# Performance work log

Hardware: AMD Instinct MI355X
Metric: run time of the kernel (lower is better)

## Reference

```python
import jax, jax.numpy as jnp
import numpy as np

H, KB = 8, 8          # z_num grid (h, k)
OB, IB = 64, 64       # per-call weight block [OB, IB, K]
K, L = 9, 9           # kernel dims of exe_unet_weight and unet_1d_weights
ZD, PD, DH = 64, 16, 128  # z_dim, pde_inputs dim, hypernet hidden


def setup_inputs() -> dict:
    key = jax.random.key(0)
    k1, k2, k3, k4, k5 = jax.random.split(key, 5)
    # z params: torch.fmod(randn, 2) as in the original __init__
    z_all = jnp.fmod(jax.random.normal(k1, (H * KB, ZD), jnp.float32), 2.0)
    W1 = jax.random.normal(k2, (DH, ZD + PD), jnp.float32) * 0.1
    b1 = jnp.zeros((DH,), jnp.float32)
    W2 = jax.random.normal(k3, (OB * IB * K, DH), jnp.float32) * 0.02
    b2 = jnp.zeros((OB * IB * K,), jnp.float32)
    unet_1d_weights = jax.random.normal(k4, (H * OB, KB * IB, L), jnp.float32)
    pde_inputs = jax.random.normal(k5, (PD,), jnp.float32)
    return {"z_all": z_all, "W1": W1, "b1": b1, "W2": W2, "b2": b2,
            "unet_1d_weights": unet_1d_weights, "pde_inputs": pde_inputs}


def reference(z_all, W1, b1, W2, b2, unet_1d_weights, pde_inputs):
    # Batched hypernet: one GEMM over all h*k z vectors instead of h*k calls.
    x = jnp.concatenate([z_all, jnp.broadcast_to(pde_inputs, (H * KB, PD))], axis=1)  # [hk, ZD+PD]
    hid = jax.nn.relu(x @ W1.T + b1)                    # [hk, DH]
    w = (hid @ W2.T + b2).reshape(H, KB, OB, IB, K)      # per-cell blocks
    # cat(dim=1) within row, cat(dim=0) across rows -> [H*OB, KB*IB, K]
    exe_unet_weight = w.transpose(0, 2, 1, 3, 4).reshape(H * OB, KB * IB, K)
    # broadcast outer product over kernel dims
    w_2d = jnp.einsum('oik,oil->oikl', exe_unet_weight, unet_1d_weights)
    return w_2d
```

## Files before the change

### kernel.cpp

```cpp
#include <hip/hip_runtime.h>

#define ZD_ 64
#define PD_ 16
#define DH_ 128
#define NW2 36864
#define HK_ 64
#define HK_TILE 8

__global__ void hid_kernel(const float* __restrict__ z_all,
                           const float* __restrict__ W1,
                           const float* __restrict__ b1,
                           const float* __restrict__ pde,
                           float* __restrict__ hid) {
    int gid = blockIdx.x * 256 + threadIdx.x;
    int r = gid >> 7;
    int d = gid & 127;
    const float* w = W1 + d * (ZD_ + PD_);
    const float* z = z_all + r * ZD_;
    float acc = b1[d];
    #pragma unroll 8
    for (int c = 0; c < ZD_; ++c) acc += z[c] * w[c];
    #pragma unroll
    for (int c = 0; c < PD_; ++c) acc += pde[c] * w[ZD_ + c];
    hid[gid] = fmaxf(acc, 0.0f);
}

__global__ void transpose_w2(const float* __restrict__ W2,
                             float* __restrict__ W2T) {
    __shared__ float s[32][33];
    int n0 = blockIdx.x * 32;
    int k0 = blockIdx.y * 32;
    int row = threadIdx.x >> 3;
    int c4  = (threadIdx.x & 7) * 4;
    float4 v = *reinterpret_cast<const float4*>(W2 + (size_t)(n0 + row) * DH_ + k0 + c4);
    s[row][c4 + 0] = v.x; s[row][c4 + 1] = v.y;
    s[row][c4 + 2] = v.z; s[row][c4 + 3] = v.w;
    __syncthreads();
    float4 w;
    w.x = s[c4 + 0][row]; w.y = s[c4 + 1][row];
    w.z = s[c4 + 2][row]; w.w = s[c4 + 3][row];
    *reinterpret_cast<float4*>(W2T + (size_t)(k0 + row) * NW2 + n0 + c4) = w;
}

__global__ void exe_kernel(const float* __restrict__ hid,
                           const float* __restrict__ W2T,
                           const float* __restrict__ b2,
                           float* __restrict__ exe) {
    int nblk = blockIdx.x % 72;
    int h    = blockIdx.x / 72;
    int n = nblk * 512 + threadIdx.x * 4;
    const float* hrow = hid + (size_t)h * HK_TILE * DH_;

    float4 bias = *reinterpret_cast<const float4*>(b2 + n);
    float4 acc[HK_TILE];
    #pragma unroll
    for (int j = 0; j < HK_TILE; ++j) acc[j] = bias;

    #pragma unroll 2
    for (int k = 0; k < DH_; k += 4) {
        float4 w0 = *reinterpret_cast<const float4*>(W2T + (size_t)(k + 0) * NW2 + n);
        float4 w1 = *reinterpret_cast<const float4*>(W2T + (size_t)(k + 1) * NW2 + n);
        float4 w2 = *reinterpret_cast<const float4*>(W2T + (size_t)(k + 2) * NW2 + n);
        float4 w3 = *reinterpret_cast<const float4*>(W2T + (size_t)(k + 3) * NW2 + n);
        #pragma unroll
        for (int j = 0; j < HK_TILE; ++j) {
            float4 hv = *reinterpret_cast<const float4*>(hrow + j * DH_ + k);
            acc[j].x += hv.x * w0.x; acc[j].y += hv.x * w0.y;
            acc[j].z += hv.x * w0.z; acc[j].w += hv.x * w0.w;
            acc[j].x += hv.y * w1.x; acc[j].y += hv.y * w1.y;
            acc[j].z += hv.y * w1.z; acc[j].w += hv.y * w1.w;
            acc[j].x += hv.z * w2.x; acc[j].y += hv.z * w2.y;
            acc[j].z += hv.z * w2.z; acc[j].w += hv.z * w2.w;
            acc[j].x += hv.w * w3.x; acc[j].y += hv.w * w3.y;
            acc[j].z += hv.w * w3.z; acc[j].w += hv.w * w3.w;
        }
    }

    int ob = n / 576;
    int r  = n % 576;
    #pragma unroll
    for (int j = 0; j < HK_TILE; ++j) {
        int o = h * 64 + ob;
        *reinterpret_cast<float4*>(exe + (size_t)o * 4608 + j * 576 + r) = acc[j];
    }
}

__global__ void outer_kernel(const float* __restrict__ exe,
                             const float* __restrict__ unet,
                             float* __restrict__ out) {
    __shared__ float s_e[576], s_u[576];
    int b = blockIdx.x;
    int o = b >> 3, c = b & 7;
    size_t base9 = (size_t)o * 4608 + (size_t)c * 576;
    const float4* e4 = reinterpret_cast<const float4*>(exe + base9);
    const float4* u4 = reinterpret_cast<const float4*>(unet + base9);
    int tid = threadIdx.x;
    if (tid < 144) {
        reinterpret_cast<float4*>(s_e)[tid] = e4[tid];
        reinterpret_cast<float4*>(s_u)[tid] = u4[tid];
    }
    __syncthreads();
    float4* o4 = reinterpret_cast<float4*>(out + (size_t)o * 41472 + (size_t)c * 5184);
    for (int idx = tid; idx < 1296; idx += 256) {
        int e0 = idx * 4;
        float4 v;
        float* vp = &v.x;
        #pragma unroll
        for (int j = 0; j < 4; ++j) {
            int e = e0 + j;
            int p = e / 81;
            int rem = e - p * 81;
            int k = rem / 9;
            int l = rem - k * 9;
            vp[j] = s_e[p * 9 + k] * s_u[p * 9 + l];
        }
        o4[idx] = v;
    }
}

extern "C" void kernel_launch(void* const* d_in, const int* in_sizes, int n_in,
                              void* d_out, int out_size, void* d_ws, size_t ws_size,
                              hipStream_t stream) {
    const float* z_all = (const float*)d_in[0];
    const float* W1    = (const float*)d_in[1];
    const float* b1    = (const float*)d_in[2];
    const float* W2    = (const float*)d_in[3];
    const float* b2    = (const float*)d_in[4];
    const float* unet  = (const float*)d_in[5];
    const float* pde   = (const float*)d_in[6];
    float* out = (float*)d_out;

    float* ws   = (float*)d_ws;
    float* hid  = ws;
    float* W2T  = ws + 8192;
    float* exe  = W2T + (size_t)DH_ * NW2;

    hid_kernel<<<32, 256, 0, stream>>>(z_all, W1, b1, pde, hid);
    transpose_w2<<<dim3(1152, 4), 256, 0, stream>>>(W2, W2T);
    exe_kernel<<<576, 128, 0, stream>>>(hid, W2T, b2, exe);
    outer_kernel<<<4096, 256, 0, stream>>>(exe, unet, out);
}
```

Baseline: 159.7 us.

## Drop W2 transpose pass; stage W2 tiles in LDS inside exe GEMM

Removes the separate transpose kernel that wrote an 18MB transposed copy of W2, and instead has each exe block load a 64-row slab of W2 into padded shared memory. Each wave computes 16 hk rows for 64 output columns, reading W2 from LDS and hid via broadcast loads. This cuts a full extra read/write pass over W2 and one launch. The trade-offs are LDS use per block, scalar rather than float4 stores to exe, and hid being re-read by every block.

```diff
diff --git a/kernel.cpp b/kernel.cpp
--- a/kernel.cpp
+++ b/kernel.cpp
@@ -3,9 +3,7 @@
 #define ZD_ 64
 #define PD_ 16
 #define DH_ 128
-#define NW2 36864
-#define HK_ 64
-#define HK_TILE 8
+#define LDS_STRIDE 132
 
 __global__ void hid_kernel(const float* __restrict__ z_all,
                            const float* __restrict__ W1,
@@ -25,63 +23,54 @@
     hid[gid] = fmaxf(acc, 0.0f);
 }
 
-__global__ void transpose_w2(const float* __restrict__ W2,
-                             float* __restrict__ W2T) {
-    __shared__ float s[32][33];
-    int n0 = blockIdx.x * 32;
-    int k0 = blockIdx.y * 32;
-    int row = threadIdx.x >> 3;
-    int c4  = (threadIdx.x & 7) * 4;
-    float4 v = *reinterpret_cast<const float4*>(W2 + (size_t)(n0 + row) * DH_ + k0 + c4);
-    s[row][c4 + 0] = v.x; s[row][c4 + 1] = v.y;
-    s[row][c4 + 2] = v.z; s[row][c4 + 3] = v.w;
+__global__ __launch_bounds__(256) void exe_kernel(
+        const float* __restrict__ hid,
+        const float* __restrict__ W2,
+        const float* __restrict__ b2,
+        float* __restrict__ exe) {
+    __shared__ __align__(16) float s_tile[64 * LDS_STRIDE];
+    int tid = threadIdx.x;
+    int n0  = blockIdx.x * 64;
+
+    const float4* g4 = reinterpret_cast<const float4*>(W2 + (size_t)n0 * DH_);
+    #pragma unroll
+    for (int j = 0; j < 8; ++j) {
+        int g  = j * 256 + tid;
+        int nl = g >> 5;
+        int k0 = (g & 31) * 4;
+        *reinterpret_cast<float4*>(&s_tile[nl * LDS_STRIDE + k0]) = g4[g];
+    }
     __syncthreads();
-    float4 w;
-    w.x = s[c4 + 0][row]; w.y = s[c4 + 1][row];
-    w.z = s[c4 + 2][row]; w.w = s[c4 + 3][row];
-    *reinterpret_cast<float4*>(W2T + (size_t)(k0 + row) * NW2 + n0 + c4) = w;
-}
 
-__global__ void exe_kernel(const float* __restrict__ hid,
-                           const float* __restrict__ W2T,
-                           const float* __restrict__ b2,
-                           float* __restrict__ exe) {
-    int nblk = blockIdx.x % 72;
-    int h    = blockIdx.x / 72;
-    int n = nblk * 512 + threadIdx.x * 4;
-    const float* hrow = hid + (size_t)h * HK_TILE * DH_;
+    int wave   = __builtin_amdgcn_readfirstlane(tid >> 6);
+    int lane   = tid & 63;
+    int hkbase = wave * 16;
+    const float* hbase = hid + (size_t)hkbase * DH_;
 
-    float4 bias = *reinterpret_cast<const float4*>(b2 + n);
-    float4 acc[HK_TILE];
+    float bias = b2[n0 + lane];
+    float acc[16];
     #pragma unroll
-    for (int j = 0; j < HK_TILE; ++j) acc[j] = bias;
+    for (int j = 0; j < 16; ++j) acc[j] = bias;
 
-    #pragma unroll 2
-    for (int k = 0; k < DH_; k += 4) {
-        float4 w0 = *reinterpret_cast<const float4*>(W2T + (size_t)(k + 0) * NW2 + n);
-        float4 w1 = *reinterpret_cast<const float4*>(W2T + (size_t)(k + 1) * NW2 + n);
-        float4 w2 = *reinterpret_cast<const float4*>(W2T + (size_t)(k + 2) * NW2 + n);
-        float4 w3 = *reinterpret_cast<const float4*>(W2T + (size_t)(k + 3) * NW2 + n);
+    const float* trow = s_tile + lane * LDS_STRIDE;
+    #pragma unroll 4
+    for (int c = 0; c < 32; ++c) {
+        int k0 = c * 4;
+        float4 v = *reinterpret_cast<const float4*>(trow + k0);
         #pragma unroll
-        for (int j = 0; j < HK_TILE; ++j) {
-            float4 hv = *reinterpret_cast<const float4*>(hrow + j * DH_ + k);
-            acc[j].x += hv.x * w0.x; acc[j].y += hv.x * w0.y;
-            acc[j].z += hv.x * w0.z; acc[j].w += hv.x * w0.w;
-            acc[j].x += hv.y * w1.x; acc[j].y += hv.y * w1.y;
-            acc[j].z += hv.y * w1.z; acc[j].w += hv.y * w1.w;
-            acc[j].x += hv.z * w2.x; acc[j].y += hv.z * w2.y;
-            acc[j].z += hv.z * w2.z; acc[j].w += hv.z * w2.w;
-            acc[j].x += hv.w * w3.x; acc[j].y += hv.w * w3.y;
-            acc[j].z += hv.w * w3.z; acc[j].w += hv.w * w3.w;
+        for (int j = 0; j < 16; ++j) {
+            float4 hv = *reinterpret_cast<const float4*>(hbase + j * DH_ + k0);
+            acc[j] += hv.x * v.x + hv.y * v.y + hv.z * v.z + hv.w * v.w;
         }
     }
 
-    int ob = n / 576;
-    int r  = n % 576;
+    int ob = n0 / 576;
+    int r  = n0 % 576 + lane;
     #pragma unroll
-    for (int j = 0; j < HK_TILE; ++j) {
-        int o = h * 64 + ob;
-        *reinterpret_cast<float4*>(exe + (size_t)o * 4608 + j * 576 + r) = acc[j];
+    for (int j = 0; j < 16; ++j) {
+        int hk = hkbase + j;
+        int h = hk >> 3, kb = hk & 7;
+        exe[(size_t)(h * 64 + ob) * 4608 + kb * 576 + r] = acc[j];
     }
 }
 
@@ -130,13 +119,11 @@
     const float* pde   = (const float*)d_in[6];
     float* out = (float*)d_out;
 
-    float* ws   = (float*)d_ws;
-    float* hid  = ws;
-    float* W2T  = ws + 8192;
-    float* exe  = W2T + (size_t)DH_ * NW2;
+    float* ws  = (float*)d_ws;
+    float* hid = ws;
+    float* exe = ws + 8192;
 
     hid_kernel<<<32, 256, 0, stream>>>(z_all, W1, b1, pde, hid);
-    transpose_w2<<<dim3(1152, 4), 256, 0, stream>>>(W2, W2T);
-    exe_kernel<<<576, 128, 0, stream>>>(hid, W2T, b2, exe);
+    exe_kernel<<<576, 256, 0, stream>>>(hid, W2, b2, exe);
     outer_kernel<<<4096, 256, 0, stream>>>(exe, unet, out);
 }
```

Result: faster. 154.7 us (-3.1%).
